# Kernel optimization log

Hardware: AMD Instinct MI355X
Metric: run time of the kernel (lower is better)

The kernel has to match this reference:

```python
import jax, jax.numpy as jnp
import numpy as np
from jax import lax

NUM_CLASSES = 5
NUM_TASKS = 20
CONV_CHANS = [(64, 3), (64, 64), (128, 64), (128, 128), (256, 128), (256, 256)]  # (out, in)


def setup_inputs() -> dict:
    key = jax.random.key(0)
    ks = jax.random.split(key, 16)
    B = 512
    x = jax.random.normal(ks[0], (B, 3, 32, 32), dtype=jnp.float32)
    tid = jax.random.randint(ks[1], (B,), 0, NUM_TASKS)
    inp = {"x": x, "tid": tid}
    for i, (oc, ic) in enumerate(CONV_CHANS):
        fan_in = ic * 9
        inp[f"w{i}"] = jax.random.normal(ks[2 + 2 * i], (oc, ic, 3, 3), dtype=jnp.float32) * np.float32((2.0 / fan_in) ** 0.5)
        inp[f"b{i}"] = jnp.zeros((oc,), dtype=jnp.float32)
    inp["cw"] = jax.random.normal(ks[14], (NUM_CLASSES * NUM_TASKS, 4096), dtype=jnp.float32) * np.float32(4096 ** -0.5)
    inp["cb"] = jnp.zeros((NUM_CLASSES * NUM_TASKS,), dtype=jnp.float32)
    return inp


def _conv_relu(x, w, b):
    y = lax.conv_general_dilated(x, w, window_strides=(1, 1), padding='SAME',
                                 dimension_numbers=('NCHW', 'OIHW', 'NCHW'))
    return jax.nn.relu(y + b[None, :, None, None])


def _maxpool2(x):
    return lax.reduce_window(x, -jnp.inf, lax.max, (1, 1, 2, 2), (1, 1, 2, 2), 'VALID')


def _forward(x, tid, ws, bs, cw, cb):
    # VGG cfg [64,64,'M',128,128,'M',256,256,'M']
    h = _conv_relu(x, ws[0], bs[0])
    h = _conv_relu(h, ws[1], bs[1])
    h = _maxpool2(h)
    h = _conv_relu(h, ws[2], bs[2])
    h = _conv_relu(h, ws[3], bs[3])
    h = _maxpool2(h)
    h = _conv_relu(h, ws[4], bs[4])
    h = _conv_relu(h, ws[5], bs[5])
    h = _maxpool2(h)                      # [B, 256, 4, 4]
    feat = h.reshape(h.shape[0], -1)      # [B, 4096], matches torch NCHW flatten
    # Batched task-indexed classifier: gather each sample's 5-row weight block.
    w_sel = cw.reshape(NUM_TASKS, NUM_CLASSES, 4096)[tid]   # [B, 5, 4096]
    b_sel = cb.reshape(NUM_TASKS, NUM_CLASSES)[tid]         # [B, 5]
    return jnp.einsum('bcd,bd->bc', w_sel, feat) + b_sel


def reference(x, tid, w0, b0, w1, b1, w2, b2, w3, b3, w4, b4, w5, b5, cw, cb):
    ws = (w0, w1, w2, w3, w4, w5)
    bs = (b0, b1, b2, b3, b4, b5)
    return _forward(x, tid, ws, bs, cw, cb)
```

## Files before the change

kernel.cpp:

```cpp
#include <hip/hip_runtime.h>


typedef __attribute__((ext_vector_type(8))) short short8;
typedef __attribute__((ext_vector_type(4))) float floatx4;
typedef unsigned int uint;
typedef unsigned short ushort;

__device__ __forceinline__ ushort f2bf(float f) {
    uint u = __float_as_uint(f);
    return (ushort)((u + 0x7fffu + ((u >> 16) & 1u)) >> 16);
}
__device__ __forceinline__ float bf2f(ushort h) {
    return __uint_as_float(((uint)h) << 16);
}

__device__ __forceinline__ void wlin_one(
    const float* __restrict__ src, short* __restrict__ dst, int OC, int IC, int o)
{
    int j    = o & 7;
    int lane = (o >> 3) & 63;
    int r    = o >> 9;
    int G16  = OC >> 4;
    int g    = r % G16;  r /= G16;
    int kk   = r % 9;
    int icb  = r / 9;
    int oc = g * 16 + (lane & 15);
    int ic = icb * 32 + (lane >> 4) * 8 + j;
    dst[o] = (short)f2bf(src[((long)oc * IC + ic) * 9 + kk]);
}

#define N_W0 2048
#define N_W1 36864
#define N_W2 73728
#define N_W3 147456
#define N_W4 294912
#define N_W5 589824
#define N_WT_TOTAL (N_W0 + N_W1 + N_W2 + N_W3 + N_W4 + N_W5)

__global__ __launch_bounds__(256) void wtransform_all(
    const float* __restrict__ w0, const float* __restrict__ w1,
    const float* __restrict__ w2, const float* __restrict__ w3,
    const float* __restrict__ w4, const float* __restrict__ w5,
    short* __restrict__ wt0, short* __restrict__ wts1, short* __restrict__ wts2,
    short* __restrict__ wts3, short* __restrict__ wts4, short* __restrict__ wts5)
{
    int idx = blockIdx.x * 256 + threadIdx.x;
    if (idx < N_W0) {
        int oc = idx >> 5, k = idx & 31;
        wt0[idx] = (k < 27) ? (short)f2bf(w0[oc * 27 + k]) : (short)0;
        return;
    }
    idx -= N_W0;
    if (idx < N_W1) { wlin_one(w1, wts1, 64, 64, idx); return; }
    idx -= N_W1;
    if (idx < N_W2) { wlin_one(w2, wts2, 128, 64, idx); return; }
    idx -= N_W2;
    if (idx < N_W3) { wlin_one(w3, wts3, 128, 128, idx); return; }
    idx -= N_W3;
    if (idx < N_W4) { wlin_one(w4, wts4, 256, 128, idx); return; }
    idx -= N_W4;
    wlin_one(w5, wts5, 256, 256, idx);
}

__global__ __launch_bounds__(256, 2) void conv0_mfma(
    const float* __restrict__ x, const short* __restrict__ wT0,
    const float* __restrict__ b0, ushort* __restrict__ out)
{
    __shared__ float  s_x[3 * 18 * 34];
    __shared__ ushort s_b[4 * 512 * 8];

    const int tid  = threadIdx.x;
    const int wv   = tid >> 6;
    const int lane = tid & 63;
    const int quad = lane >> 4;
    const int l16  = lane & 15;
    const int b    = blockIdx.x >> 1;
    const int r0   = (blockIdx.x & 1) * 16;

    for (int idx = tid; idx < 3 * 18 * 34; idx += 256) {
        int c   = idx / 612;
        int rem = idx - c * 612;
        int ry  = rem / 34, rx = rem - ry * 34;
        int gy  = r0 + ry - 1, gx = rx - 1;
        float v = 0.f;
        if (gy >= 0 && gy < 32 && gx >= 0 && gx < 32)
            v = x[(((long)b * 3 + c) * 32 + gy) * 32 + gx];
        s_x[idx] = v;
    }
    __syncthreads();

#pragma unroll
    for (int rep = 0; rep < 2; ++rep) {
        int pxl = rep * 256 + tid;
        int py = pxl >> 5, px = pxl & 31;
        ushort v[32];
#pragma unroll
        for (int c = 0; c < 3; ++c)
#pragma unroll
            for (int ky = 0; ky < 3; ++ky)
#pragma unroll
                for (int kx = 0; kx < 3; ++kx)
                    v[c * 9 + ky * 3 + kx] = f2bf(s_x[c * 612 + (py + ky) * 34 + (px + kx)]);
#pragma unroll
        for (int k = 27; k < 32; ++k) v[k] = 0;
#pragma unroll
        for (int q = 0; q < 4; ++q)
            *(uint4*)(&s_b[(q * 512 + pxl) * 8]) = *(const uint4*)(v + q * 8);
    }
    __syncthreads();

    floatx4 acc[4][8];
#pragma unroll
    for (int i = 0; i < 4; ++i)
#pragma unroll
        for (int t = 0; t < 8; ++t) acc[i][t] = (floatx4)0.f;

    short8 afr[4];
#pragma unroll
    for (int i = 0; i < 4; ++i)
        afr[i] = *(const short8*)(wT0 + (i * 16 + l16) * 32 + quad * 8);
#pragma unroll
    for (int t = 0; t < 8; ++t) {
        int pxl = wv * 128 + t * 16 + l16;
        short8 bfr = *(const short8*)(&s_b[(quad * 512 + pxl) * 8]);
#pragma unroll
        for (int i = 0; i < 4; ++i)
            acc[i][t] = __builtin_amdgcn_mfma_f32_16x16x32_bf16(afr[i], bfr, acc[i][t], 0, 0, 0);
    }

#pragma unroll
    for (int i = 0; i < 4; ++i) {
        int oc0 = i * 16 + quad * 4;
        float4 bv = *(const float4*)(b0 + oc0);
#pragma unroll
        for (int t = 0; t < 8; ++t) {
            int pxl = wv * 128 + t * 16 + l16;
            int py = pxl >> 5, px = pxl & 31;
            long dst = ((((long)b * 8 + (oc0 >> 3)) * 32 + r0 + py) * 32 + px) * 8 + (oc0 & 7);
            float v0 = acc[i][t][0] + bv.x;
            float v1 = acc[i][t][1] + bv.y;
            float v2 = acc[i][t][2] + bv.z;
            float v3 = acc[i][t][3] + bv.w;
            ushort o[4];
            o[0] = f2bf(v0 > 0.f ? v0 : 0.f);
            o[1] = f2bf(v1 > 0.f ? v1 : 0.f);
            o[2] = f2bf(v2 > 0.f ? v2 : 0.f);
            o[3] = f2bf(v3 > 0.f ? v3 : 0.f);
            *(uint2*)(out + dst) = *(uint2*)o;
        }
    }
}

template<int IC, int OC, int H, int W, int ROWS, int OCGROUPS, bool POOL>
__global__ __launch_bounds__(256, 3) void conv_so(
    const ushort* __restrict__ act_in,
    const short*  __restrict__ wTs,
    const float*  __restrict__ bias,
    ushort* __restrict__ act_out)
{
    constexpr int WPAD  = W + 2;
    constexpr int RPAD  = ROWS + 2;
    constexpr int UNITS = RPAD * WPAD;
    constexpr int SEGS  = H / ROWS;
    constexpr int C8I   = IC / 8;
    constexpr int CPUP  = C8I + 1;
    constexpr int G16   = OC / 16;
    constexpr int NICB  = IC / 32;
    constexpr int C8O   = OC / 8;
    constexpr int TMAX  = NICB * 9;

    __shared__ ushort s_act[UNITS * CPUP * 8];

    const int tid  = threadIdx.x;
    const int wv   = tid >> 6;
    const int lane = tid & 63;
    const int quad = lane >> 4;
    const int l16  = lane & 15;

    const int b   = blockIdx.x / SEGS;
    const int seg = blockIdx.x - b * SEGS;
    const int r0  = seg * ROWS;
    const int ocg = wv % OCGROUPS;
    const int pxg = wv / OCGROUPS;

    for (int c = tid; c < UNITS * C8I; c += 256) {
        int sub  = c / UNITS;
        int unit = c - sub * UNITS;
        int ry   = unit / WPAD, cx = unit - ry * WPAD;
        int gy   = r0 + ry - 1, gx = cx - 1;
        uint4 val = make_uint4(0, 0, 0, 0);
        if ((unsigned)gy < (unsigned)H && (unsigned)gx < (unsigned)W) {
            long src = ((((long)b * C8I + sub) * H + gy) * W + gx) * 8;
            val = *(const uint4*)(act_in + src);
        }
        *(uint4*)(&s_act[((size_t)unit * CPUP + sub) * 8]) = val;
    }
    __syncthreads();

    floatx4 acc[4][4];
#pragma unroll
    for (int i = 0; i < 4; ++i)
#pragma unroll
        for (int t = 0; t < 4; ++t) acc[i][t] = (floatx4)0.f;

    int bbase[4];
#pragma unroll
    for (int t = 0; t < 4; ++t) {
        int pxl = pxg * 64 + t * 16 + l16;
        int py  = pxl / W, px = pxl - py * W;
        bbase[t] = (py * WPAD + px) * CPUP * 8;
    }

    const short8* wb = (const short8*)wTs;
    const int  wbase = (ocg * 4) * 64 + lane;
    const long WSTEP = (long)G16 * 64;

    short8 wpipe[3][4];
#pragma unroll
    for (int d = 0; d < 3; ++d)
#pragma unroll
        for (int i = 0; i < 4; ++i)
            wpipe[d][i] = wb[(long)d * WSTEP + wbase + i * 64];

    int tl = 0;
    for (int icb = 0; icb < NICB; ++icb) {
#pragma unroll
        for (int kk = 0; kk < 9; ++kk) {
            const int ky = kk / 3, kx = kk - ky * 3;
            const int koff = ((ky * WPAD + kx) * CPUP + quad) * 8 + icb * 32;
            short8 bfr[4];
#pragma unroll
            for (int t = 0; t < 4; ++t)
                bfr[t] = *(const short8*)(&s_act[bbase[t] + koff]);
            const int slot = kk % 3;
#pragma unroll
            for (int i = 0; i < 4; ++i)
#pragma unroll
                for (int t = 0; t < 4; ++t)
                    acc[i][t] = __builtin_amdgcn_mfma_f32_16x16x32_bf16(
                        wpipe[slot][i], bfr[t], acc[i][t], 0, 0, 0);
            int tn = tl + 3;
            if (tn >= TMAX) tn = 0;
#pragma unroll
            for (int i = 0; i < 4; ++i)
                wpipe[slot][i] = wb[(long)tn * WSTEP + wbase + i * 64];
            ++tl;
        }
    }

    if constexpr (!POOL) {
#pragma unroll
        for (int i = 0; i < 4; ++i) {
            int oc0 = ocg * 64 + i * 16 + quad * 4;
            float4 bv = *(const float4*)(bias + oc0);
#pragma unroll
            for (int t = 0; t < 4; ++t) {
                int pxl = pxg * 64 + t * 16 + l16;
                int py  = pxl / W, px = pxl - py * W;
                long dst = ((((long)b * C8O + (oc0 >> 3)) * H + r0 + py) * W + px) * 8 + (oc0 & 7);
                float v0 = acc[i][t][0] + bv.x;
                float v1 = acc[i][t][1] + bv.y;
                float v2 = acc[i][t][2] + bv.z;
                float v3 = acc[i][t][3] + bv.w;
                ushort o[4];
                o[0] = f2bf(v0 > 0.f ? v0 : 0.f);
                o[1] = f2bf(v1 > 0.f ? v1 : 0.f);
                o[2] = f2bf(v2 > 0.f ? v2 : 0.f);
                o[3] = f2bf(v3 > 0.f ? v3 : 0.f);
                *(uint2*)(act_out + dst) = *(uint2*)o;
            }
        }
    } else {
        __syncthreads();
        ushort* s_pool = s_act;
        constexpr int PSTR = OC + 8;
        static_assert(ROWS * W * PSTR <= UNITS * CPUP * 8, "pool scratch fits");
#pragma unroll
        for (int i = 0; i < 4; ++i) {
            int oc0 = ocg * 64 + i * 16 + quad * 4;
            float4 bv = *(const float4*)(bias + oc0);
#pragma unroll
            for (int t = 0; t < 4; ++t) {
                int pxl = pxg * 64 + t * 16 + l16;
                float v0 = acc[i][t][0] + bv.x;
                float v1 = acc[i][t][1] + bv.y;
                float v2 = acc[i][t][2] + bv.z;
                float v3 = acc[i][t][3] + bv.w;
                ushort o[4];
                o[0] = f2bf(v0 > 0.f ? v0 : 0.f);
                o[1] = f2bf(v1 > 0.f ? v1 : 0.f);
                o[2] = f2bf(v2 > 0.f ? v2 : 0.f);
                o[3] = f2bf(v3 > 0.f ? v3 : 0.f);
                *(uint2*)(&s_pool[pxl * PSTR + oc0]) = *(uint2*)o;
            }
        }
        __syncthreads();
        constexpr int PH = ROWS / 2, PW = W / 2, HOT = H / 2;
        const int pr0 = r0 / 2;
        for (int u = tid; u < PH * PW * C8O; u += 256) {
            int c8 = u % C8O;
            int pp = u / C8O;
            int xo = pp % PW, yo = pp / PW;
            const ushort* p00 = &s_pool[((2 * yo) * W + 2 * xo) * PSTR + c8 * 8];
            uint4 q0 = *(const uint4*)(p00);
            uint4 q1 = *(const uint4*)(p00 + PSTR);
            uint4 q2 = *(const uint4*)(p00 + W * PSTR);
            uint4 q3 = *(const uint4*)(p00 + W * PSTR + PSTR);
            const ushort* a0 = (const ushort*)&q0;
            const ushort* a1 = (const ushort*)&q1;
            const ushort* a2 = (const ushort*)&q2;
            const ushort* a3 = (const ushort*)&q3;
            ushort r[8];
#pragma unroll
            for (int j = 0; j < 8; ++j) {
                ushort m0 = a0[j] > a1[j] ? a0[j] : a1[j];
                ushort m1 = a2[j] > a3[j] ? a2[j] : a3[j];
                r[j] = m0 > m1 ? m0 : m1;
            }
            long dst = ((((long)b * C8O + c8) * HOT + pr0 + yo) * PW + xo) * 8;
            *(uint4*)(act_out + dst) = *(uint4*)r;
        }
    }
}

__global__ __launch_bounds__(256) void classifier_k(
    const ushort* __restrict__ feat, const int* __restrict__ tids,
    const float* __restrict__ cw, const float* __restrict__ cb,
    float* __restrict__ out, int B)
{
    int g = blockIdx.x * 256 + threadIdx.x;
    int wid = g >> 6, lane = g & 63;
    if (wid >= B * 5) return;
    int b = wid / 5, c = wid - b * 5;
    int t = tids[b];
    const float* wrow = cw + (long)(t * 5 + c) * 4096;
    const ushort* f = feat + (long)b * 4096;
    float s = 0.f;
#pragma unroll 4
    for (int d = lane; d < 4096; d += 64) {
        int fidx = (((d >> 7) * 16) + (d & 15)) * 8 + ((d >> 4) & 7);
        s += wrow[d] * bf2f(f[fidx]);
    }
#pragma unroll
    for (int off = 32; off > 0; off >>= 1) s += __shfl_down(s, off, 64);
    if (lane == 0) out[wid] = s + cb[t * 5 + c];
}

extern "C" void kernel_launch(void* const* d_in, const int* in_sizes, int n_in,
                              void* d_out, int out_size, void* d_ws, size_t ws_size,
                              hipStream_t stream)
{
    const float* x   = (const float*)d_in[0];
    const int*   tid = (const int*)d_in[1];
    const float* w0 = (const float*)d_in[2];  const float* b0 = (const float*)d_in[3];
    const float* w1 = (const float*)d_in[4];  const float* b1 = (const float*)d_in[5];
    const float* w2 = (const float*)d_in[6];  const float* b2 = (const float*)d_in[7];
    const float* w3 = (const float*)d_in[8];  const float* b3 = (const float*)d_in[9];
    const float* w4 = (const float*)d_in[10]; const float* b4 = (const float*)d_in[11];
    const float* w5 = (const float*)d_in[12]; const float* b5 = (const float*)d_in[13];
    const float* cw = (const float*)d_in[14];
    const float* cb = (const float*)d_in[15];
    float* outp = (float*)d_out;

    const int B = in_sizes[0] / (3 * 32 * 32);

    short* wt0  = (short*)d_ws;
    short* wts1 = wt0 + N_W0;
    short* wts2 = wts1 + N_W1;
    short* wts3 = wts2 + N_W2;
    short* wts4 = wts3 + N_W3;
    short* wts5 = wts4 + N_W4;
    const size_t WT_HW = N_WT_TOTAL;
    const size_t fixed_bytes = WT_HW * 2;

    int Bc = B;
    while (Bc > 2 && fixed_bytes + (size_t)Bc * 2 * 65536 * 2 > ws_size) Bc >>= 1;
    if (Bc < 2) Bc = 2;

    ushort* bufA = (ushort*)((short*)d_ws + WT_HW);
    ushort* bufB = bufA + (size_t)Bc * 65536;

    wtransform_all<<<(N_WT_TOTAL + 255) / 256, 256, 0, stream>>>(
        w0, w1, w2, w3, w4, w5, wt0, wts1, wts2, wts3, wts4, wts5);

    for (int cb0 = 0; cb0 < B; cb0 += Bc) {
        const float* xc = x + (size_t)cb0 * 3 * 32 * 32;
        const int* tidc = tid + cb0;
        float* outc = outp + (size_t)cb0 * 5;

        conv0_mfma<<<Bc * 2, 256, 0, stream>>>(xc, wt0, b0, bufA);
        conv_so<64, 64, 32, 32, 8, 1, true><<<Bc * 4, 256, 0, stream>>>(bufA, wts1, b1, bufB);
        conv_so<64, 128, 16, 16, 8, 2, false><<<Bc * 2, 256, 0, stream>>>(bufB, wts2, b2, bufA);
        conv_so<128, 128, 16, 16, 8, 2, true><<<Bc * 2, 256, 0, stream>>>(bufA, wts3, b3, bufB);
        conv_so<128, 256, 8, 8, 8, 4, false><<<Bc, 256, 0, stream>>>(bufB, wts4, b4, bufA);
        conv_so<256, 256, 8, 8, 8, 4, true><<<Bc, 256, 0, stream>>>(bufA, wts5, b5, bufB);
        classifier_k<<<(Bc * 5 * 64 + 255) / 256, 256, 0, stream>>>(bufB, tidc, cw, cb, outc, Bc);
    }
}
```

Measured before the change: 285.6 us.

## Stage conv activations into LDS via direct global_load_lds with channel-major layout

```diff
diff --git a/kernel.cpp b/kernel.cpp
--- a/kernel.cpp
+++ b/kernel.cpp
@@ -12,6 +12,12 @@
 }
 __device__ __forceinline__ float bf2f(ushort h) {
     return __uint_as_float(((uint)h) << 16);
+}
+
+typedef const __attribute__((address_space(1))) unsigned int* gas_ptr;
+typedef __attribute__((address_space(3))) unsigned int* las_ptr;
+__device__ __forceinline__ void gload_lds16(const void* g, void* l) {
+    __builtin_amdgcn_global_load_lds((gas_ptr)g, (las_ptr)l, 16, 0, 0);
 }
 
 __device__ __forceinline__ void wlin_one(
@@ -42,8 +48,10 @@
     const float* __restrict__ w2, const float* __restrict__ w3,
     const float* __restrict__ w4, const float* __restrict__ w5,
     short* __restrict__ wt0, short* __restrict__ wts1, short* __restrict__ wts2,
-    short* __restrict__ wts3, short* __restrict__ wts4, short* __restrict__ wts5)
-{
+    short* __restrict__ wts3, short* __restrict__ wts4, short* __restrict__ wts5,
+    short* __restrict__ zp)
+{
+    if (blockIdx.x == 0 && threadIdx.x < 32) zp[threadIdx.x] = 0;
     int idx = blockIdx.x * 256 + threadIdx.x;
     if (idx < N_W0) {
         int oc = idx >> 5, k = idx & 31;
@@ -156,20 +164,21 @@
     const ushort* __restrict__ act_in,
     const short*  __restrict__ wTs,
     const float*  __restrict__ bias,
-    ushort* __restrict__ act_out)
+    ushort* __restrict__ act_out,
+    const ushort* __restrict__ zp)
 {
     constexpr int WPAD  = W + 2;
     constexpr int RPAD  = ROWS + 2;
     constexpr int UNITS = RPAD * WPAD;
     constexpr int SEGS  = H / ROWS;
     constexpr int C8I   = IC / 8;
-    constexpr int CPUP  = C8I + 1;
     constexpr int G16   = OC / 16;
     constexpr int NICB  = IC / 32;
     constexpr int C8O   = OC / 8;
     constexpr int TMAX  = NICB * 9;
-
-    __shared__ ushort s_act[UNITS * CPUP * 8];
+    constexpr int NSTG  = UNITS * C8I;
+
+    __shared__ ushort s_act[NSTG * 8];
 
     const int tid  = threadIdx.x;
     const int wv   = tid >> 6;
@@ -183,17 +192,15 @@
     const int ocg = wv % OCGROUPS;
     const int pxg = wv / OCGROUPS;
 
-    for (int c = tid; c < UNITS * C8I; c += 256) {
+    for (int c = tid; c < NSTG; c += 256) {
         int sub  = c / UNITS;
         int unit = c - sub * UNITS;
         int ry   = unit / WPAD, cx = unit - ry * WPAD;
         int gy   = r0 + ry - 1, gx = cx - 1;
-        uint4 val = make_uint4(0, 0, 0, 0);
-        if ((unsigned)gy < (unsigned)H && (unsigned)gx < (unsigned)W) {
-            long src = ((((long)b * C8I + sub) * H + gy) * W + gx) * 8;
-            val = *(const uint4*)(act_in + src);
-        }
-        *(uint4*)(&s_act[((size_t)unit * CPUP + sub) * 8]) = val;
+        const ushort* src = zp;
+        if ((unsigned)gy < (unsigned)H && (unsigned)gx < (unsigned)W)
+            src = act_in + ((((long)b * C8I + sub) * H + gy) * W + gx) * 8;
+        gload_lds16(src, &s_act[(size_t)(c - lane) * 8]);
     }
     __syncthreads();
 
@@ -208,7 +215,7 @@
     for (int t = 0; t < 4; ++t) {
         int pxl = pxg * 64 + t * 16 + l16;
         int py  = pxl / W, px = pxl - py * W;
-        bbase[t] = (py * WPAD + px) * CPUP * 8;
+        bbase[t] = (py * WPAD + px) * 8;
     }
 
     const short8* wb = (const short8*)wTs;
@@ -227,7 +234,7 @@
 #pragma unroll
         for (int kk = 0; kk < 9; ++kk) {
             const int ky = kk / 3, kx = kk - ky * 3;
-            const int koff = ((ky * WPAD + kx) * CPUP + quad) * 8 + icb * 32;
+            const int koff = ((icb * 4 + quad) * UNITS + ky * WPAD + kx) * 8;
             short8 bfr[4];
 #pragma unroll
             for (int t = 0; t < 4; ++t)
@@ -274,7 +281,7 @@
         __syncthreads();
         ushort* s_pool = s_act;
         constexpr int PSTR = OC + 8;
-        static_assert(ROWS * W * PSTR <= UNITS * CPUP * 8, "pool scratch fits");
+        static_assert(ROWS * W * PSTR <= NSTG * 8, "pool scratch fits");
 #pragma unroll
         for (int i = 0; i < 4; ++i) {
             int oc0 = ocg * 64 + i * 16 + quad * 4;
@@ -370,7 +377,8 @@
     short* wts3 = wts2 + N_W2;
     short* wts4 = wts3 + N_W3;
     short* wts5 = wts4 + N_W4;
-    const size_t WT_HW = N_WT_TOTAL;
+    short* zp   = wts5 + N_W5;
+    const size_t WT_HW = (size_t)N_WT_TOTAL + 32;
     const size_t fixed_bytes = WT_HW * 2;
 
     int Bc = B;
@@ -381,7 +389,7 @@
     ushort* bufB = bufA + (size_t)Bc * 65536;
 
     wtransform_all<<<(N_WT_TOTAL + 255) / 256, 256, 0, stream>>>(
-        w0, w1, w2, w3, w4, w5, wt0, wts1, wts2, wts3, wts4, wts5);
+        w0, w1, w2, w3, w4, w5, wt0, wts1, wts2, wts3, wts4, wts5, zp);
 
     for (int cb0 = 0; cb0 < B; cb0 += Bc) {
         const float* xc = x + (size_t)cb0 * 3 * 32 * 32;
@@ -389,11 +397,11 @@
         float* outc = outp + (size_t)cb0 * 5;
 
         conv0_mfma<<<Bc * 2, 256, 0, stream>>>(xc, wt0, b0, bufA);
-        conv_so<64, 64, 32, 32, 8, 1, true><<<Bc * 4, 256, 0, stream>>>(bufA, wts1, b1, bufB);
-        conv_so<64, 128, 16, 16, 8, 2, false><<<Bc * 2, 256, 0, stream>>>(bufB, wts2, b2, bufA);
-        conv_so<128, 128, 16, 16, 8, 2, true><<<Bc * 2, 256, 0, stream>>>(bufA, wts3, b3, bufB);
-        conv_so<128, 256, 8, 8, 8, 4, false><<<Bc, 256, 0, stream>>>(bufB, wts4, b4, bufA);
-        conv_so<256, 256, 8, 8, 8, 4, true><<<Bc, 256, 0, stream>>>(bufA, wts5, b5, bufB);
+        conv_so<64, 64, 32, 32, 8, 1, true><<<Bc * 4, 256, 0, stream>>>(bufA, wts1, b1, bufB, (ushort*)zp);
+        conv_so<64, 128, 16, 16, 8, 2, false><<<Bc * 2, 256, 0, stream>>>(bufB, wts2, b2, bufA, (ushort*)zp);
+        conv_so<128, 128, 16, 16, 8, 2, true><<<Bc * 2, 256, 0, stream>>>(bufA, wts3, b3, bufB, (ushort*)zp);
+        conv_so<128, 256, 8, 8, 8, 4, false><<<Bc, 256, 0, stream>>>(bufB, wts4, b4, bufA, (ushort*)zp);
+        conv_so<256, 256, 8, 8, 8, 4, true><<<Bc, 256, 0, stream>>>(bufA, wts5, b5, bufB, (ushort*)zp);
         classifier_k<<<(Bc * 5 * 64 + 255) / 256, 256, 0, stream>>>(bufB, tidc, cw, cb, outc, Bc);
     }
 }
```

Measured after the change: 268.0 us. -6.2%, faster.
